# Kernel optimization log

Measured on AMD Instinct MI355X. Metric: run time of the kernel, lower is better.

## Reference

```python
import jax, jax.numpy as jnp
import numpy as np
import math

DIM = 512
HEADS = 8
DIM_HEAD = 64
SCALE = math.sqrt(DIM_HEAD)
EPS = 1e-12


def rms_norm(x, g):
    # F.normalize(x, dim=1) * g * sqrt(dim); x: [B, C, H, W], g: [C]
    inv = jax.lax.rsqrt(jnp.sum(x * x, axis=1, keepdims=True) + EPS)
    return x * inv * g[None, :, None, None] * jnp.asarray(math.sqrt(x.shape[1]), x.dtype)


def setup_inputs() -> dict:
    key = jax.random.key(0)
    k1, k2, k3 = jax.random.split(key, 3)
    B, H, W = 8, 64, 64
    hidden = HEADS * DIM_HEAD
    x = jax.random.normal(k1, (B, DIM, H, W), dtype=jnp.float32)
    w_qkv = jax.random.normal(k2, (3 * hidden, DIM), dtype=jnp.float32) * (1.0 / math.sqrt(DIM))
    w_out = jax.random.normal(k3, (DIM, hidden), dtype=jnp.float32) * (1.0 / math.sqrt(hidden))
    b_out = jnp.zeros((DIM,), dtype=jnp.float32)
    g1 = jnp.ones((DIM,), dtype=jnp.float32)
    g2 = jnp.ones((DIM,), dtype=jnp.float32)
    return {"x": x, "g1": g1, "w_qkv": w_qkv, "w_out": w_out, "b_out": b_out, "g2": g2}


def reference(x, g1, w_qkv, w_out, b_out, g2):
    B, C, H, W = x.shape
    n = H * W
    xn = rms_norm(x, g1)
    # 1x1 conv == channel matmul: [B, 3*hidden, H, W]
    qkv = jnp.einsum('bchw,oc->bohw', xn, w_qkv)
    q, k, v = jnp.split(qkv, 3, axis=1)
    # b (h c) x y -> b h c n
    def to_heads(t):
        return t.reshape(B, HEADS, DIM_HEAD, n)
    q, k, v = to_heads(q), to_heads(k), to_heads(v)
    q = jax.nn.softmax(q, axis=2) / SCALE   # softmax over channel dim d
    k = jax.nn.softmax(k, axis=3)           # softmax over spatial dim n
    context = jnp.einsum('bhdn,bhen->bhde', k, v)   # [B, H, d, e]
    out = jnp.einsum('bhde,bhdn->bhen', context, q) # [B, H, e, n]
    out = out.reshape(B, HEADS * DIM_HEAD, H, W)
    out = jnp.einsum('bchw,oc->bohw', out, w_out) + b_out[None, :, None, None]
    return rms_norm(out, g2)
```

## Files before the change

kernel.cpp:

```cpp
#include <hip/hip_runtime.h>


typedef unsigned short u16;
typedef __attribute__((ext_vector_type(8))) short short8;
typedef __attribute__((ext_vector_type(4))) short short4_t;
typedef __attribute__((ext_vector_type(4))) float f32x4;

static constexpr size_t XN_B = (size_t)512 * 4096;
static constexpr size_t KV_B = (size_t)1024 * 4096;
static constexpr float SQRT512 = 22.62741699796952f;

typedef const __attribute__((address_space(1))) unsigned int gu32;
typedef __attribute__((address_space(3))) unsigned int lu32;

__device__ __forceinline__ float b2f(u16 u){
  union { unsigned u; float f; } x; x.u = ((unsigned)u) << 16; return x.f;
}
__device__ __forceinline__ u16 f2b(float f){
  union { float f; unsigned u; } x; x.f = f;
  unsigned r = x.u + 0x7FFFu + ((x.u >> 16) & 1u);
  return (u16)(r >> 16);
}
__device__ __forceinline__ void gl16(const u16* g, u16* l){
  __builtin_amdgcn_global_load_lds((gu32*)g, (lu32*)l, 16, 0, 0);
}

__global__ __launch_bounds__(256)
void kcvt(const float* __restrict__ wqkv, const float* __restrict__ wout,
          const float* __restrict__ g1, u16* __restrict__ dq, u16* __restrict__ dw){
  size_t i = ((size_t)blockIdx.x * 256 + threadIdx.x) * 4;
  short4_t o;
  if (i < (size_t)786432){
    f32x4 v = *(const f32x4*)(wqkv + i);
    int c = (int)(i & 511);
    #pragma unroll
    for (int j = 0; j < 4; j++) o[j] = (short)f2b(v[j] * g1[c + j] * SQRT512);
    *(short4_t*)(dq + i) = o;
  } else {
    size_t off = i - 786432;
    f32x4 v = *(const f32x4*)(wout + off);
    #pragma unroll
    for (int j = 0; j < 4; j++) o[j] = (short)f2b(v[j]);
    *(short4_t*)(dw + off) = o;
  }
}

__global__ __launch_bounds__(256)
void krms1(const float* __restrict__ x, u16* __restrict__ xnT){
  __shared__ u16 lt[32][514];
  __shared__ float red[256];
  __shared__ float invs[32];
  int t = threadIdx.x;
  int pg0 = blockIdx.x * 32;
  int b = pg0 >> 12, p0 = pg0 & 4095;
  int px = t & 31, chunk = t >> 5;
  const float* xp = x + (size_t)b * XN_B + p0 + px;
  float s = 0.f;
  #pragma unroll 4
  for (int c = chunk * 64; c < chunk * 64 + 64; ++c){
    float v = xp[(size_t)c * 4096];
    lt[px][c] = f2b(v);
    s += v * v;
  }
  red[t] = s;
  __syncthreads();
  if (chunk == 0){
    float tt = red[px] + red[px + 32] + red[px + 64] + red[px + 96]
             + red[px + 128] + red[px + 160] + red[px + 192] + red[px + 224];
    invs[px] = rsqrtf(tt + 1e-12f);
  }
  __syncthreads();
  int px2 = t >> 3, c0 = (t & 7) * 8;
  float iv = invs[px2];
  u16* dst = xnT + (size_t)(pg0 + px2) * 512;
  #pragma unroll
  for (int j = 0; j < 8; j++){
    int c = c0 + j * 64;
    short8 o;
    #pragma unroll
    for (int e = 0; e < 8; e++) o[e] = (short)f2b(b2f(lt[px2][c + e]) * iv);
    *(short8*)(dst + c) = o;
  }
}

template<int ADD_BIAS, int SMAX>
__global__ __launch_bounds__(512)
void gemm_big(const u16* __restrict__ Ab, long astr, int lda,
              const u16* __restrict__ Bb, long bstr, int ldb,
              u16* __restrict__ Cb, long cstr, int ldc,
              const float* __restrict__ bias)
{
  constexpr int NT = 16;
  const u16* A  = Ab + (size_t)blockIdx.z * astr;
  const u16* BT = Bb + (size_t)blockIdx.z * bstr;
  u16* C = Cb + (size_t)blockIdx.z * cstr;
  const int m0 = blockIdx.y * 256, n0 = blockIdx.x * 256;
  __shared__ u16 As[2][256 * 32];
  __shared__ u16 Bs[2][256 * 32];
  const int tid = threadIdx.x;
  const int lane = tid & 63, wid = tid >> 6;
  const int wr = (wid >> 2) * 128, wc = (wid & 3) * 64;
  const int fr = lane & 15, fq = lane >> 4;
  const int srow = tid >> 2;
  const int sslot = tid & 3;
  f32x4 acc[8][4] = {};

  auto STAGE = [&](int s, int t){
    const int k0 = t * 32;
    #pragma unroll
    for (int r = 0; r < 2; r++){
      int row = r * 128 + srow;
      int gj = (sslot ^ ((row >> 1) & 3)) * 8;
      gl16(A  + (size_t)(m0 + row) * lda + k0 + gj, &As[s][0] + r * 4096 + tid * 8);
      gl16(BT + (size_t)(n0 + row) * ldb + k0 + gj, &Bs[s][0] + r * 4096 + tid * 8);
    }
  };

  STAGE(0, 0);
  int cur = 0;
  for (int t = 0; t < NT; t++){
    if (t + 1 < NT){
      STAGE(cur ^ 1, t + 1);
      asm volatile("s_waitcnt vmcnt(4)" ::: "memory");
    } else {
      asm volatile("s_waitcnt vmcnt(0)" ::: "memory");
    }
    __builtin_amdgcn_s_barrier();
    __builtin_amdgcn_sched_barrier(0);
    short8 a[8], b[4];
    #pragma unroll
    for (int i = 0; i < 8; i++){
      int ra = wr + i * 16 + fr;
      a[i] = *(const short8*)(&As[cur][0] + ra * 32 + ((fq ^ ((ra >> 1) & 3)) * 8));
    }
    #pragma unroll
    for (int j = 0; j < 4; j++){
      int rb = wc + j * 16 + fr;
      b[j] = *(const short8*)(&Bs[cur][0] + rb * 32 + ((fq ^ ((rb >> 1) & 3)) * 8));
    }
    __builtin_amdgcn_s_setprio(1);
    #pragma unroll
    for (int i = 0; i < 8; i++)
      #pragma unroll
      for (int j = 0; j < 4; j++)
        acc[i][j] = __builtin_amdgcn_mfma_f32_16x16x32_bf16(a[i], b[j], acc[i][j], 0, 0, 0);
    __builtin_amdgcn_s_setprio(0);
    __builtin_amdgcn_sched_barrier(0);
    __builtin_amdgcn_s_barrier();
    cur ^= 1;
  }

  if constexpr (SMAX){
    #pragma unroll
    for (int i = 0; i < 8; i++)
      #pragma unroll
      for (int e = 0; e < 4; e++){
        float mx = fmaxf(fmaxf(acc[i][0][e], acc[i][1][e]),
                         fmaxf(acc[i][2][e], acc[i][3][e]));
        mx = fmaxf(mx, __shfl_xor(mx, 1));
        mx = fmaxf(mx, __shfl_xor(mx, 2));
        mx = fmaxf(mx, __shfl_xor(mx, 4));
        mx = fmaxf(mx, __shfl_xor(mx, 8));
        float p0 = __expf(acc[i][0][e] - mx);
        float p1 = __expf(acc[i][1][e] - mx);
        float p2 = __expf(acc[i][2][e] - mx);
        float p3 = __expf(acc[i][3][e] - mx);
        float s = p0 + p1 + p2 + p3;
        s += __shfl_xor(s, 1);
        s += __shfl_xor(s, 2);
        s += __shfl_xor(s, 4);
        s += __shfl_xor(s, 8);
        float r = 1.f / (s * 8.0f);
        acc[i][0][e] = p0 * r; acc[i][1][e] = p1 * r;
        acc[i][2][e] = p2 * r; acc[i][3][e] = p3 * r;
      }
  }
  #pragma unroll
  for (int i = 0; i < 8; i++)
    #pragma unroll
    for (int j = 0; j < 4; j++)
      #pragma unroll
      for (int e = 0; e < 4; e++){
        int row = m0 + wr + i * 16 + fq * 4 + e;
        int col = n0 + wc + j * 16 + fr;
        float v = acc[i][j][e];
        if constexpr (ADD_BIAS) v += bias[col];
        C[(size_t)row * ldc + col] = f2b(v);
      }
}

__global__ __launch_bounds__(256)
void kstats(const u16* __restrict__ kv, float* __restrict__ stats){
  int bx = blockIdx.x;
  int b = bx >> 9, c = bx & 511;
  const u16* kp = kv + (size_t)b * KV_B + (size_t)c * 4096;
  int tid = threadIdx.x;
  float v[16], mx = -1e30f;
  #pragma unroll
  for (int j = 0; j < 2; j++){
    short8 t = *(const short8*)(kp + j * 2048 + tid * 8);
    #pragma unroll
    for (int e = 0; e < 8; e++){ v[j * 8 + e] = b2f((u16)t[e]); mx = fmaxf(mx, v[j * 8 + e]); }
  }
  #pragma unroll
  for (int o = 32; o >= 1; o >>= 1) mx = fmaxf(mx, __shfl_xor(mx, o));
  __shared__ float redm[4], reds[4];
  if ((tid & 63) == 0) redm[tid >> 6] = mx;
  __syncthreads();
  mx = fmaxf(fmaxf(redm[0], redm[1]), fmaxf(redm[2], redm[3]));
  float s = 0.f;
  #pragma unroll
  for (int j = 0; j < 16; j++) s += __expf(v[j] - mx);
  #pragma unroll
  for (int o = 32; o >= 1; o >>= 1) s += __shfl_xor(s, o);
  if ((tid & 63) == 0) reds[tid >> 6] = s;
  __syncthreads();
  if (tid == 0){
    float st = reds[0] + reds[1] + reds[2] + reds[3];
    stats[bx] = mx;
    stats[4096 + bx] = 1.f / st;
  }
}

__global__ __launch_bounds__(256)
void gemm_ctx(const u16* __restrict__ kv, float* __restrict__ P,
              const float* __restrict__ stats)
{
  constexpr int K = 1024;
  const int z = blockIdx.z;
  const int tid = threadIdx.x;
  const int ar = tid >> 2, ac = (tid & 3) * 8;
  int bh = z >> 2, sp = z & 3, b = bh >> 3, h = bh & 7;
  const u16* A  = kv + (size_t)b * KV_B + (size_t)(h * 64) * 4096 + sp * 1024;
  const u16* BT = kv + (size_t)b * KV_B + (size_t)(512 + h * 64) * 4096 + sp * 1024;
  int sidx = b * 512 + h * 64 + ar;
  float mxr = stats[sidx], rsr = stats[4096 + sidx];
  __shared__ u16 As[64 * 40];
  __shared__ u16 Bs[64 * 40];
  const int wid = tid >> 6, lane = tid & 63;
  const int wr = (wid >> 1) * 32, wc = (wid & 1) * 32;
  const int lr = lane & 15, kb = lane >> 4;
  f32x4 acc[2][2] = {};
  for (int k0 = 0; k0 < K; k0 += 32){
    short8 av = *(const short8*)(A + (size_t)ar * 4096 + k0 + ac);
    short8 ao;
    #pragma unroll
    for (int e = 0; e < 8; e++)
      ao[e] = (short)f2b(__expf(b2f((u16)av[e]) - mxr) * rsr);
    *(short8*)(As + ar * 40 + ac) = ao;
    *(short8*)(Bs + ar * 40 + ac) = *(const short8*)(BT + (size_t)ar * 4096 + k0 + ac);
    __syncthreads();
    short8 a0 = *(const short8*)(As + (wr +      lr) * 40 + kb * 8);
    short8 a1 = *(const short8*)(As + (wr + 16 + lr) * 40 + kb * 8);
    short8 b0 = *(const short8*)(Bs + (wc +      lr) * 40 + kb * 8);
    short8 b1 = *(const short8*)(Bs + (wc + 16 + lr) * 40 + kb * 8);
    acc[0][0] = __builtin_amdgcn_mfma_f32_16x16x32_bf16(a0, b0, acc[0][0], 0, 0, 0);
    acc[0][1] = __builtin_amdgcn_mfma_f32_16x16x32_bf16(a0, b1, acc[0][1], 0, 0, 0);
    acc[1][0] = __builtin_amdgcn_mfma_f32_16x16x32_bf16(a1, b0, acc[1][0], 0, 0, 0);
    acc[1][1] = __builtin_amdgcn_mfma_f32_16x16x32_bf16(a1, b1, acc[1][1], 0, 0, 0);
    __syncthreads();
  }
  #pragma unroll
  for (int mi = 0; mi < 2; mi++)
    #pragma unroll
    for (int ni = 0; ni < 2; ni++)
      #pragma unroll
      for (int j = 0; j < 4; j++){
        int row = wr + mi * 16 + kb * 4 + j;
        int col = wc + ni * 16 + lr;
        P[(size_t)z * 4096 + (size_t)row * 64 + col] = acc[mi][ni][j];
      }
}

__global__ __launch_bounds__(256)
void kreduce(const float* __restrict__ P, u16* __restrict__ ctxD){
  int o = blockIdx.x * 256 + threadIdx.x;
  int bh = o >> 12, r = o & 4095;
  const float* p = P + ((size_t)bh << 14) + r;
  float s = p[0] + p[4096] + p[8192] + p[12288];
  ctxD[((size_t)bh << 12) + r] = f2b(s);
}

__global__ __launch_bounds__(256)
void gemm_ctxw(const u16* __restrict__ woutbf, const u16* __restrict__ ctxD,
               u16* __restrict__ M)
{
  const int z = blockIdx.z;
  const int b = z >> 3, h = z & 7;
  const int m0 = blockIdx.y * 64;
  const u16* A  = woutbf + h * 64;
  const u16* BT = ctxD + (size_t)z * 4096;
  const int tid = threadIdx.x;
  const int ar = tid >> 2, ac = (tid & 3) * 8;
  __shared__ u16 As[64 * 40];
  __shared__ u16 Bs[64 * 40];
  const int wid = tid >> 6, lane = tid & 63;
  const int wr = (wid >> 1) * 32, wc = (wid & 1) * 32;
  const int lr = lane & 15, kb = lane >> 4;
  f32x4 acc[2][2] = {};
  for (int k0 = 0; k0 < 64; k0 += 32){
    *(short8*)(As + ar * 40 + ac) = *(const short8*)(A + (size_t)(m0 + ar) * 512 + k0 + ac);
    *(short8*)(Bs + ar * 40 + ac) = *(const short8*)(BT + (size_t)ar * 64 + k0 + ac);
    __syncthreads();
    short8 a0 = *(const short8*)(As + (wr +      lr) * 40 + kb * 8);
    short8 a1 = *(const short8*)(As + (wr + 16 + lr) * 40 + kb * 8);
    short8 b0 = *(const short8*)(Bs + (wc +      lr) * 40 + kb * 8);
    short8 b1 = *(const short8*)(Bs + (wc + 16 + lr) * 40 + kb * 8);
    acc[0][0] = __builtin_amdgcn_mfma_f32_16x16x32_bf16(a0, b0, acc[0][0], 0, 0, 0);
    acc[0][1] = __builtin_amdgcn_mfma_f32_16x16x32_bf16(a0, b1, acc[0][1], 0, 0, 0);
    acc[1][0] = __builtin_amdgcn_mfma_f32_16x16x32_bf16(a1, b0, acc[1][0], 0, 0, 0);
    acc[1][1] = __builtin_amdgcn_mfma_f32_16x16x32_bf16(a1, b1, acc[1][1], 0, 0, 0);
    __syncthreads();
  }
  #pragma unroll
  for (int mi = 0; mi < 2; mi++)
    #pragma unroll
    for (int ni = 0; ni < 2; ni++)
      #pragma unroll
      for (int j = 0; j < 4; j++){
        int row = m0 + wr + mi * 16 + kb * 4 + j;
        int col = wc + ni * 16 + lr;
        M[(size_t)b * 262144 + (size_t)row * 512 + h * 64 + col] = f2b(acc[mi][ni][j]);
      }
}

__global__ __launch_bounds__(256)
void krms2(const u16* __restrict__ o2, const float* __restrict__ g,
           float* __restrict__ out){
  __shared__ u16 lt[32][514];
  __shared__ float invs[32];
  __shared__ float gl[512];
  int t = threadIdx.x;
  int pg0 = blockIdx.x * 32;
  int b = pg0 >> 12, p0 = pg0 & 4095;
  gl[t] = g[t] * SQRT512;
  gl[t + 256] = g[t + 256] * SQRT512;
  int px2 = t >> 3, c0 = (t & 7) * 8;
  const u16* src = o2 + (size_t)(pg0 + px2) * 512;
  float s = 0.f;
  #pragma unroll
  for (int j = 0; j < 8; j++){
    int c = c0 + j * 64;
    short8 v = *(const short8*)(src + c);
    *(short8*)&lt[px2][c] = v;
    #pragma unroll
    for (int e = 0; e < 8; e++){ float f = b2f((u16)v[e]); s += f * f; }
  }
  s += __shfl_xor(s, 1); s += __shfl_xor(s, 2); s += __shfl_xor(s, 4);
  if ((t & 7) == 0) invs[px2] = rsqrtf(s + 1e-12f);
  __syncthreads();
  int c2 = t >> 2, pxc = (t & 3) * 8;
  float ivv[8];
  #pragma unroll
  for (int e = 0; e < 8; e++) ivv[e] = invs[pxc + e];
  #pragma unroll
  for (int pass = 0; pass < 8; pass++){
    int c = c2 + pass * 64;
    float gf = gl[c];
    float* dst = out + ((size_t)(b * 512 + c)) * 4096 + p0 + pxc;
    #pragma unroll
    for (int q = 0; q < 2; q++){
      f32x4 o;
      #pragma unroll
      for (int e = 0; e < 4; e++){
        int pp = q * 4 + e;
        o[e] = b2f(lt[pxc + pp][c]) * ivv[pp] * gf;
      }
      *(f32x4*)(dst + q * 4) = o;
    }
  }
}

extern "C" void kernel_launch(void* const* d_in, const int* in_sizes, int n_in,
                              void* d_out, int out_size, void* d_ws, size_t ws_size,
                              hipStream_t stream)
{
  (void)in_sizes; (void)n_in; (void)out_size; (void)ws_size;
  const float* x    = (const float*)d_in[0];
  const float* g1   = (const float*)d_in[1];
  const float* wqkv = (const float*)d_in[2];
  const float* wout = (const float*)d_in[3];
  const float* bout = (const float*)d_in[4];
  const float* g2   = (const float*)d_in[5];
  float* out = (float*)d_out;
  char* ws = (char*)d_ws;

  u16*   xnT   = (u16*)(ws);
  float* P     = (float*)(ws);
  u16*   M     = (u16*)(ws + (size_t)8388608);
  u16*   qT    = (u16*)(ws + (size_t)33554432);
  u16*   kv    = (u16*)(ws + (size_t)67108864);
  u16*   out2T = (u16*)(ws + (size_t)67108864);
  u16*   wbf   = (u16*)(ws + (size_t)134217728);
  u16*   ctxD  = (u16*)(ws + (size_t)134217728);
  float* stats = (float*)(ws + (size_t)134742016);
  u16*   wkvbf = wbf + (size_t)512 * 512;
  u16*   woutbf= (u16*)(ws + (size_t)135790592);

  kcvt<<<1024, 256, 0, stream>>>(wqkv, wout, g1, wbf, woutbf);
  krms1<<<1024, 256, 0, stream>>>(x, xnT);
  gemm_big<0, 1><<<dim3(2, 128, 1), 512, 0, stream>>>(xnT, 0, 512, wbf, 0, 512,
                                                      qT, 0, 512, nullptr);
  gemm_big<0, 0><<<dim3(16, 4, 8), 512, 0, stream>>>(wkvbf, 0, 512,
                                                     xnT, (long)4096 * 512, 512,
                                                     kv, (long)KV_B, 4096, nullptr);
  kstats<<<4096, 256, 0, stream>>>(kv, stats);
  gemm_ctx<<<dim3(1, 1, 256), 256, 0, stream>>>(kv, P, stats);
  kreduce<<<1024, 256, 0, stream>>>(P, ctxD);
  gemm_ctxw<<<dim3(1, 8, 64), 256, 0, stream>>>(woutbf, ctxD, M);
  gemm_big<1, 0><<<dim3(2, 16, 8), 512, 0, stream>>>(qT, (long)4096 * 512, 512,
                                                     M, (long)262144, 512,
                                                     out2T, (long)4096 * 512, 512, bout);
  krms2<<<1024, 256, 0, stream>>>(out2T, g2, out);
}
```

Baseline: 198.1 us.

## Fuse softmax stats into KV GEMM epilogue and merge small kernels

```diff
diff --git a/kernel.cpp b/kernel.cpp
--- a/kernel.cpp
+++ b/kernel.cpp
@@ -26,32 +26,33 @@
 }
 
 __global__ __launch_bounds__(256)
-void kcvt(const float* __restrict__ wqkv, const float* __restrict__ wout,
-          const float* __restrict__ g1, u16* __restrict__ dq, u16* __restrict__ dw){
-  size_t i = ((size_t)blockIdx.x * 256 + threadIdx.x) * 4;
-  short4_t o;
-  if (i < (size_t)786432){
-    f32x4 v = *(const f32x4*)(wqkv + i);
-    int c = (int)(i & 511);
-    #pragma unroll
-    for (int j = 0; j < 4; j++) o[j] = (short)f2b(v[j] * g1[c + j] * SQRT512);
-    *(short4_t*)(dq + i) = o;
-  } else {
-    size_t off = i - 786432;
-    f32x4 v = *(const f32x4*)(wout + off);
-    #pragma unroll
-    for (int j = 0; j < 4; j++) o[j] = (short)f2b(v[j]);
-    *(short4_t*)(dw + off) = o;
-  }
-}
-
-__global__ __launch_bounds__(256)
-void krms1(const float* __restrict__ x, u16* __restrict__ xnT){
+void kprep(const float* __restrict__ wqkv, const float* __restrict__ wout,
+           const float* __restrict__ g1, u16* __restrict__ dq, u16* __restrict__ dw,
+           const float* __restrict__ x, u16* __restrict__ xnT){
   __shared__ u16 lt[32][514];
   __shared__ float red[256];
   __shared__ float invs[32];
+  int bid = blockIdx.x;
   int t = threadIdx.x;
-  int pg0 = blockIdx.x * 32;
+  if (bid < 1024){
+    size_t i = ((size_t)bid * 256 + t) * 4;
+    short4_t o;
+    if (i < (size_t)786432){
+      f32x4 v = *(const f32x4*)(wqkv + i);
+      int c = (int)(i & 511);
+      #pragma unroll
+      for (int j = 0; j < 4; j++) o[j] = (short)f2b(v[j] * g1[c + j] * SQRT512);
+      *(short4_t*)(dq + i) = o;
+    } else {
+      size_t off = i - 786432;
+      f32x4 v = *(const f32x4*)(wout + off);
+      #pragma unroll
+      for (int j = 0; j < 4; j++) o[j] = (short)f2b(v[j]);
+      *(short4_t*)(dw + off) = o;
+    }
+    return;
+  }
+  int pg0 = (bid - 1024) * 32;
   int b = pg0 >> 12, p0 = pg0 & 4095;
   int px = t & 31, chunk = t >> 5;
   const float* xp = x + (size_t)b * XN_B + p0 + px;
@@ -190,36 +191,92 @@
 }
 
 __global__ __launch_bounds__(256)
-void kstats(const u16* __restrict__ kv, float* __restrict__ stats){
-  int bx = blockIdx.x;
-  int b = bx >> 9, c = bx & 511;
-  const u16* kp = kv + (size_t)b * KV_B + (size_t)c * 4096;
-  int tid = threadIdx.x;
-  float v[16], mx = -1e30f;
-  #pragma unroll
-  for (int j = 0; j < 2; j++){
-    short8 t = *(const short8*)(kp + j * 2048 + tid * 8);
-    #pragma unroll
-    for (int e = 0; e < 8; e++){ v[j * 8 + e] = b2f((u16)t[e]); mx = fmaxf(mx, v[j * 8 + e]); }
-  }
-  #pragma unroll
-  for (int o = 32; o >= 1; o >>= 1) mx = fmaxf(mx, __shfl_xor(mx, o));
-  __shared__ float redm[4], reds[4];
-  if ((tid & 63) == 0) redm[tid >> 6] = mx;
-  __syncthreads();
-  mx = fmaxf(fmaxf(redm[0], redm[1]), fmaxf(redm[2], redm[3]));
-  float s = 0.f;
-  #pragma unroll
-  for (int j = 0; j < 16; j++) s += __expf(v[j] - mx);
-  #pragma unroll
-  for (int o = 32; o >= 1; o >>= 1) s += __shfl_xor(s, o);
-  if ((tid & 63) == 0) reds[tid >> 6] = s;
-  __syncthreads();
-  if (tid == 0){
-    float st = reds[0] + reds[1] + reds[2] + reds[3];
-    stats[bx] = mx;
-    stats[4096 + bx] = 1.f / st;
-  }
+void gemm_kv(const u16* __restrict__ Wkv, const u16* __restrict__ xnT,
+             u16* __restrict__ kvb, float* __restrict__ stats)
+{
+  constexpr int NT = 8;
+  const int z = blockIdx.z;
+  const u16* A  = Wkv;
+  const u16* BT = xnT + (size_t)z * XN_B;
+  u16* C = kvb + (size_t)z * KV_B;
+  const int m0 = blockIdx.y * 128, n0 = blockIdx.x * 128;
+  __shared__ u16 As[2][128 * 64];
+  __shared__ u16 Bs[2][128 * 64];
+  const int tid = threadIdx.x;
+  const int srow0 = tid >> 3;
+  const int schunk = tid & 7;
+  const int lane = tid & 63, wid = tid >> 6;
+  const int wr = (wid >> 1) * 64, wc = (wid & 1) * 64;
+  const int fr = lane & 15, fq = lane >> 4;
+  f32x4 acc[4][4] = {};
+
+  auto STAGE = [&](int s, int t){
+    const int k0 = t * 64;
+    #pragma unroll
+    for (int r = 0; r < 4; r++){
+      int row = r * 32 + srow0;
+      int gj = (schunk ^ (row & 7)) * 8;
+      gl16(A  + (size_t)(m0 + row) * 512 + k0 + gj, &As[s][0] + r * 2048 + tid * 8);
+      gl16(BT + (size_t)(n0 + row) * 512 + k0 + gj, &Bs[s][0] + r * 2048 + tid * 8);
+    }
+  };
+
+  STAGE(0, 0);
+  int cur = 0;
+  for (int t = 0; t < NT; t++){
+    if (t + 1 < NT){
+      STAGE(cur ^ 1, t + 1);
+      asm volatile("s_waitcnt vmcnt(8)" ::: "memory");
+    } else {
+      asm volatile("s_waitcnt vmcnt(0)" ::: "memory");
+    }
+    __builtin_amdgcn_s_barrier();
+    __builtin_amdgcn_sched_barrier(0);
+    #pragma unroll
+    for (int ks = 0; ks < 2; ks++){
+      short8 a[4], b[4];
+      #pragma unroll
+      for (int i = 0; i < 4; i++){
+        int ra = wr + i * 16 + fr;
+        a[i] = *(const short8*)(&As[cur][0] + ra * 64 + ((ks * 4 + fq) ^ (ra & 7)) * 8);
+        int rb = wc + i * 16 + fr;
+        b[i] = *(const short8*)(&Bs[cur][0] + rb * 64 + ((ks * 4 + fq) ^ (rb & 7)) * 8);
+      }
+      __builtin_amdgcn_s_setprio(1);
+      #pragma unroll
+      for (int i = 0; i < 4; i++)
+        #pragma unroll
+        for (int j = 0; j < 4; j++)
+          acc[i][j] = __builtin_amdgcn_mfma_f32_16x16x32_bf16(a[i], b[j], acc[i][j], 0, 0, 0);
+      __builtin_amdgcn_s_setprio(0);
+    }
+    __builtin_amdgcn_sched_barrier(0);
+    __builtin_amdgcn_s_barrier();
+    cur ^= 1;
+  }
+
+  const bool krows = (m0 < 512);
+  #pragma unroll
+  for (int i = 0; i < 4; i++)
+    #pragma unroll
+    for (int e = 0; e < 4; e++){
+      int row = m0 + wr + i * 16 + fq * 4 + e;
+      float s = 0.f;
+      #pragma unroll
+      for (int j = 0; j < 4; j++){
+        int col = n0 + wc + j * 16 + fr;
+        u16 vc = f2b(acc[i][j][e]);
+        C[(size_t)row * 4096 + col] = vc;
+        if (krows) s += __expf(b2f(vc));
+      }
+      if (krows){
+        s += __shfl_xor(s, 1);
+        s += __shfl_xor(s, 2);
+        s += __shfl_xor(s, 4);
+        s += __shfl_xor(s, 8);
+        if (fr == 0) atomicAdd(stats + z * 512 + row, s);
+      }
+    }
 }
 
 __global__ __launch_bounds__(256)
@@ -233,8 +290,7 @@
   int bh = z >> 2, sp = z & 3, b = bh >> 3, h = bh & 7;
   const u16* A  = kv + (size_t)b * KV_B + (size_t)(h * 64) * 4096 + sp * 1024;
   const u16* BT = kv + (size_t)b * KV_B + (size_t)(512 + h * 64) * 4096 + sp * 1024;
-  int sidx = b * 512 + h * 64 + ar;
-  float mxr = stats[sidx], rsr = stats[4096 + sidx];
+  float rsr = 1.f / stats[b * 512 + h * 64 + ar];
   __shared__ u16 As[64 * 40];
   __shared__ u16 Bs[64 * 40];
   const int wid = tid >> 6, lane = tid & 63;
@@ -246,7 +302,7 @@
     short8 ao;
     #pragma unroll
     for (int e = 0; e < 8; e++)
-      ao[e] = (short)f2b(__expf(b2f((u16)av[e]) - mxr) * rsr);
+      ao[e] = (short)f2b(__expf(b2f((u16)av[e])) * rsr);
     *(short8*)(As + ar * 40 + ac) = ao;
     *(short8*)(Bs + ar * 40 + ac) = *(const short8*)(BT + (size_t)ar * 4096 + k0 + ac);
     __syncthreads();
@@ -273,44 +329,42 @@
 }
 
 __global__ __launch_bounds__(256)
-void kreduce(const float* __restrict__ P, u16* __restrict__ ctxD){
-  int o = blockIdx.x * 256 + threadIdx.x;
-  int bh = o >> 12, r = o & 4095;
-  const float* p = P + ((size_t)bh << 14) + r;
-  float s = p[0] + p[4096] + p[8192] + p[12288];
-  ctxD[((size_t)bh << 12) + r] = f2b(s);
-}
-
-__global__ __launch_bounds__(256)
-void gemm_ctxw(const u16* __restrict__ woutbf, const u16* __restrict__ ctxD,
-               u16* __restrict__ M)
+void kctxw(const float* __restrict__ P, const u16* __restrict__ woutbf,
+           u16* __restrict__ M)
 {
   const int z = blockIdx.z;
   const int b = z >> 3, h = z & 7;
   const int m0 = blockIdx.y * 64;
-  const u16* A  = woutbf + h * 64;
-  const u16* BT = ctxD + (size_t)z * 4096;
   const int tid = threadIdx.x;
-  const int ar = tid >> 2, ac = (tid & 3) * 8;
-  __shared__ u16 As[64 * 40];
-  __shared__ u16 Bs[64 * 40];
+  __shared__ u16 As[64 * 72];
+  __shared__ u16 Bs[64 * 72];
+  {
+    int r = tid >> 2, c0 = (tid & 3) * 16;
+    const u16* wsrc = woutbf + (size_t)(m0 + r) * 512 + h * 64 + c0;
+    *(short8*)(As + r * 72 + c0)     = *(const short8*)(wsrc);
+    *(short8*)(As + r * 72 + c0 + 8) = *(const short8*)(wsrc + 8);
+    const float* p = P + (size_t)z * 16384 + (size_t)r * 64 + c0;
+    #pragma unroll
+    for (int e = 0; e < 16; e++){
+      float s = p[e] + p[e + 4096] + p[e + 8192] + p[e + 12288];
+      Bs[r * 72 + c0 + e] = f2b(s);
+    }
+  }
+  __syncthreads();
   const int wid = tid >> 6, lane = tid & 63;
   const int wr = (wid >> 1) * 32, wc = (wid & 1) * 32;
   const int lr = lane & 15, kb = lane >> 4;
   f32x4 acc[2][2] = {};
+  #pragma unroll
   for (int k0 = 0; k0 < 64; k0 += 32){
-    *(short8*)(As + ar * 40 + ac) = *(const short8*)(A + (size_t)(m0 + ar) * 512 + k0 + ac);
-    *(short8*)(Bs + ar * 40 + ac) = *(const short8*)(BT + (size_t)ar * 64 + k0 + ac);
-    __syncthreads();
-    short8 a0 = *(const short8*)(As + (wr +      lr) * 40 + kb * 8);
-    short8 a1 = *(const short8*)(As + (wr + 16 + lr) * 40 + kb * 8);
-    short8 b0 = *(const short8*)(Bs + (wc +      lr) * 40 + kb * 8);
-    short8 b1 = *(const short8*)(Bs + (wc + 16 + lr) * 40 + kb * 8);
+    short8 a0 = *(const short8*)(As + (wr +      lr) * 72 + k0 + kb * 8);
+    short8 a1 = *(const short8*)(As + (wr + 16 + lr) * 72 + k0 + kb * 8);
+    short8 b0 = *(const short8*)(Bs + (wc +      lr) * 72 + k0 + kb * 8);
+    short8 b1 = *(const short8*)(Bs + (wc + 16 + lr) * 72 + k0 + kb * 8);
     acc[0][0] = __builtin_amdgcn_mfma_f32_16x16x32_bf16(a0, b0, acc[0][0], 0, 0, 0);
     acc[0][1] = __builtin_amdgcn_mfma_f32_16x16x32_bf16(a0, b1, acc[0][1], 0, 0, 0);
     acc[1][0] = __builtin_amdgcn_mfma_f32_16x16x32_bf16(a1, b0, acc[1][0], 0, 0, 0);
     acc[1][1] = __builtin_amdgcn_mfma_f32_16x16x32_bf16(a1, b1, acc[1][1], 0, 0, 0);
-    __syncthreads();
   }
   #pragma unroll
   for (int mi = 0; mi < 2; mi++)
@@ -392,22 +446,17 @@
   u16*   kv    = (u16*)(ws + (size_t)67108864);
   u16*   out2T = (u16*)(ws + (size_t)67108864);
   u16*   wbf   = (u16*)(ws + (size_t)134217728);
-  u16*   ctxD  = (u16*)(ws + (size_t)134217728);
-  float* stats = (float*)(ws + (size_t)134742016);
   u16*   wkvbf = wbf + (size_t)512 * 512;
   u16*   woutbf= (u16*)(ws + (size_t)135790592);
-
-  kcvt<<<1024, 256, 0, stream>>>(wqkv, wout, g1, wbf, woutbf);
-  krms1<<<1024, 256, 0, stream>>>(x, xnT);
+  float* stats = (float*)(ws + (size_t)136314880);
+
+  hipMemsetAsync(stats, 0, 4096 * sizeof(float), stream);
+  kprep<<<2048, 256, 0, stream>>>(wqkv, wout, g1, wbf, woutbf, x, xnT);
   gemm_big<0, 1><<<dim3(2, 128, 1), 512, 0, stream>>>(xnT, 0, 512, wbf, 0, 512,
                                                       qT, 0, 512, nullptr);
-  gemm_big<0, 0><<<dim3(16, 4, 8), 512, 0, stream>>>(wkvbf, 0, 512,
-                                                     xnT, (long)4096 * 512, 512,
-                                                     kv, (long)KV_B, 4096, nullptr);
-  kstats<<<4096, 256, 0, stream>>>(kv, stats);
+  gemm_kv<<<dim3(32, 8, 8), 256, 0, stream>>>(wkvbf, xnT, kv, stats);
   gemm_ctx<<<dim3(1, 1, 256), 256, 0, stream>>>(kv, P, stats);
-  kreduce<<<1024, 256, 0, stream>>>(P, ctxD);
-  gemm_ctxw<<<dim3(1, 8, 64), 256, 0, stream>>>(woutbf, ctxD, M);
+  kctxw<<<dim3(1, 8, 64), 256, 0, stream>>>(P, woutbf, M);
   gemm_big<1, 0><<<dim3(2, 16, 8), 512, 0, stream>>>(qT, (long)4096 * 512, 512,
                                                      M, (long)262144, 512,
                                                      out2T, (long)4096 * 512, 512, bout);
```

New measurement: 198.8 us. Within noise of the previous version (+0.3%).
